# Performance work log

Hardware: AMD Instinct MI355X
Metric: run time of the kernel (lower is better)

Reference implementation:

```python
import jax, jax.numpy as jnp
import numpy as np

N_HEAD = 8
HEAD_DIM = 64
DIM = 512
INNER = N_HEAD * HEAD_DIM
ATT_THRESHOLD = 1e-4
SCALE = HEAD_DIM ** -0.5


def setup_inputs() -> dict:
    key = jax.random.key(0)
    ks = jax.random.split(key, 7)
    b, n, dn = 2, 2048, 2048
    fr = jax.random.normal(ks[0], (b, n, DIM), dtype=jnp.float32)
    dt = jax.random.normal(ks[1], (b, dn, DIM), dtype=jnp.float32)
    s = DIM ** -0.5
    Wq = jax.random.normal(ks[2], (DIM, INNER), dtype=jnp.float32) * s
    Wk = jax.random.normal(ks[3], (DIM, INNER), dtype=jnp.float32) * s
    Wv = jax.random.normal(ks[4], (DIM, INNER), dtype=jnp.float32) * s
    Wo = jax.random.normal(ks[5], (INNER, DIM), dtype=jnp.float32) * (INNER ** -0.5)
    bo = jax.random.normal(ks[6], (DIM,), dtype=jnp.float32) * 0.01
    return {"fr": fr, "dt": dt, "Wq": Wq, "Wk": Wk, "Wv": Wv, "Wo": Wo, "bo": bo}


def reference(fr, dt, Wq, Wk, Wv, Wo, bo):
    b, n, _ = fr.shape
    dn = dt.shape[1]
    # projections -> [b, seq, n_head, head_dim]
    q = (fr @ Wq).reshape(b, n, N_HEAD, HEAD_DIM)
    k = (dt @ Wk).reshape(b, dn, N_HEAD, HEAD_DIM)
    v = (dt @ Wv).reshape(b, dn, N_HEAD, HEAD_DIM)
    # full attention matrix [b, h, n, dn]
    scores = jnp.einsum('bihd,bjhd->bhij', q, k) * SCALE
    attn = jax.nn.softmax(scores, axis=-1)
    # torch .clip(t) with one positional arg clamps the MIN: max(attn, t)
    attn = jnp.maximum(attn, ATT_THRESHOLD) - ATT_THRESHOLD
    attn = attn / jnp.sum(attn, axis=-1, keepdims=True)
    out = jnp.einsum('bhij,bjhd->bihd', attn, v).reshape(b, n, INNER)
    return out @ Wo + bo
```

## Files before the change

kernel.cpp:

```cpp
#include <hip/hip_runtime.h>
#include <hip/hip_bf16.h>

#define BB 2
#define SEQ 2048
#define NHEAD 8
#define HD 64
#define ATT_T 1e-4f
#define QSCALE 0.18033688011112042f

typedef short s16x8 __attribute__((ext_vector_type(8)));
typedef float f32x16 __attribute__((ext_vector_type(16)));

#define MFMA32(a, b, c) __builtin_amdgcn_mfma_f32_32x32x16_bf16((a), (b), (c), 0, 0, 0)
#define EXP2(x) __builtin_amdgcn_exp2f(x)
#define SB0() __builtin_amdgcn_sched_barrier(0)
#define WAITVM0() __builtin_amdgcn_s_waitcnt(0x0F70)
#define WAITVM4() __builtin_amdgcn_s_waitcnt(0x0F74)
#define WAITVM8() __builtin_amdgcn_s_waitcnt(0x0F78)

__device__ __forceinline__ unsigned short bfr(float x) {
  __hip_bfloat16 h = __float2bfloat16(x);
  return __builtin_bit_cast(unsigned short, h);
}
__device__ __forceinline__ unsigned int packbf(float a, float b) {
  return (unsigned int)bfr(a) | ((unsigned int)bfr(b) << 16);
}
__device__ __forceinline__ unsigned int permpack(float a, float b) {
  return __builtin_amdgcn_perm(__builtin_bit_cast(unsigned int, b),
                               __builtin_bit_cast(unsigned int, a), 0x07060302u);
}
__device__ __forceinline__ void async16(const void* g, void* l) {
  __builtin_amdgcn_global_load_lds(
      (const __attribute__((address_space(1))) unsigned int*)g,
      (__attribute__((address_space(3))) unsigned int*)l, 16, 0, 0);
}
__device__ __forceinline__ void plswap(unsigned a, unsigned b, int lh,
                                       unsigned& x, unsigned& z) {
#if __has_builtin(__builtin_amdgcn_permlane32_swap)
  typedef unsigned uint2v __attribute__((ext_vector_type(2)));
  uint2v r = __builtin_amdgcn_permlane32_swap(a, b, false, false);
  x = r[0];
  z = r[1];
#else
  unsigned ea = (unsigned)__shfl_xor((int)a, 32);
  unsigned eb = (unsigned)__shfl_xor((int)b, 32);
  x = lh ? eb : a;
  z = lh ? b : ea;
#endif
}

__global__ __launch_bounds__(256) void convT(const float* __restrict__ w0,
                                             const float* __restrict__ w1,
                                             const float* __restrict__ w2,
                                             const float* __restrict__ w3,
                                             unsigned short* __restrict__ o0,
                                             unsigned short* __restrict__ o1,
                                             unsigned short* __restrict__ o2,
                                             unsigned short* __restrict__ o3) {
  __shared__ float tle[64][65];
  const float* W = blockIdx.z == 0 ? w0 : blockIdx.z == 1 ? w1 : blockIdx.z == 2 ? w2 : w3;
  unsigned short* WT = blockIdx.z == 0 ? o0 : blockIdx.z == 1 ? o1 : blockIdx.z == 2 ? o2 : o3;
  const int r0 = blockIdx.y * 64, c0 = blockIdx.x * 64;
  const int tr = threadIdx.x >> 4;
  const int tc = threadIdx.x & 15;
  #pragma unroll
  for (int i = 0; i < 4; i++) {
    int r = tr + i * 16;
    float4 v = *(const float4*)(W + (size_t)(r0 + r) * 512 + c0 + tc * 4);
    tle[r][tc * 4 + 0] = v.x;
    tle[r][tc * 4 + 1] = v.y;
    tle[r][tc * 4 + 2] = v.z;
    tle[r][tc * 4 + 3] = v.w;
  }
  __syncthreads();
  #pragma unroll
  for (int i = 0; i < 4; i++) {
    int c = tr + i * 16;
    int rr = tc * 4;
    uint2 p;
    p.x = packbf(tle[rr + 0][c], tle[rr + 1][c]);
    p.y = packbf(tle[rr + 2][c], tle[rr + 3][c]);
    *(uint2*)(WT + (size_t)(c0 + c) * 512 + r0 + rr) = p;
  }
}

__global__ __launch_bounds__(256) void gemm_qkv(const float* __restrict__ frF,
                                                const float* __restrict__ dtF,
                                                const unsigned short* __restrict__ WqT,
                                                const unsigned short* __restrict__ WkT,
                                                const unsigned short* __restrict__ WvT,
                                                unsigned short* __restrict__ Qp,
                                                unsigned short* __restrict__ Kp,
                                                unsigned short* __restrict__ VTp) {
  __shared__ __align__(16) unsigned short smem[24576];
  unsigned short* Asm = smem;
  unsigned short* Bsm = smem + 8192;
  const int tid = threadIdx.x, lane = tid & 63, w = tid >> 6;
  const int l31 = lane & 31, lh = lane >> 5;
  const int m0 = blockIdx.y * 64, n0 = blockIdx.x * 128;
  const int z = blockIdx.z;
  const float* A = z == 0 ? frF : dtF;
  const unsigned short* BT = z == 0 ? WqT : (z == 1 ? WkT : WvT);
  unsigned short* OP = z == 0 ? Qp : (z == 1 ? Kp : VTp);
  const float scale = z == 0 ? QSCALE : 1.0f;

  const int arow = tid >> 2, aseg = tid & 3;
  const float* Ap = A + (size_t)(m0 + arow) * 512 + aseg * 16;
  const int aoff = (arow >> 5) * 2048 + aseg * 512 + (arow & 31) * 8;

  auto stageB = [&](int kt, int buf) {
    const int k0 = kt * 64;
    #pragma unroll
    for (int i = 0; i < 4; i++) {
      int r = w * 4 + i, gn = r >> 2, ks = r & 3;
      async16(BT + (size_t)(n0 + gn * 32 + l31) * 512 + k0 + ks * 16 + lh * 8,
              Bsm + buf * 8192 + r * 512);
    }
  };
  auto ldA = [&](int kt, float4* r4) {
    #pragma unroll
    for (int i = 0; i < 4; i++) r4[i] = *(const float4*)(Ap + kt * 64 + i * 4);
  };
  auto wrA = [&](int buf, const float4* r4) {
    uint4 w0v, w1v;
    w0v.x = packbf(r4[0].x, r4[0].y); w0v.y = packbf(r4[0].z, r4[0].w);
    w0v.z = packbf(r4[1].x, r4[1].y); w0v.w = packbf(r4[1].z, r4[1].w);
    w1v.x = packbf(r4[2].x, r4[2].y); w1v.y = packbf(r4[2].z, r4[2].w);
    w1v.z = packbf(r4[3].x, r4[3].y); w1v.w = packbf(r4[3].z, r4[3].w);
    *(uint4*)(Asm + buf * 4096 + aoff) = w0v;
    *(uint4*)(Asm + buf * 4096 + aoff + 256) = w1v;
  };

  f32x16 acc[2];
  #pragma unroll
  for (int j = 0; j < 2; j++)
    #pragma unroll
    for (int r = 0; r < 16; r++) acc[j][r] = 0.f;

  float4 areg[4];
  ldA(0, areg);
  stageB(0, 0);
  wrA(0, areg);
  ldA(1, areg);

  for (int kt = 0; kt < 8; ++kt) {
    __syncthreads();
    if (kt + 1 < 8) {
      const int nb = (kt + 1) & 1;
      stageB(kt + 1, nb);
      wrA(nb, areg);
      if (kt + 2 < 8) ldA(kt + 2, areg);
    }
    const int buf = kt & 1;
    const unsigned short* as = Asm + buf * 4096 + (w & 1) * 2048;
    const unsigned short* bs = Bsm + buf * 8192 + (w >> 1) * 4096;
    #pragma unroll
    for (int ks = 0; ks < 4; ++ks) {
      s16x8 af = *(const s16x8*)(as + ks * 512 + lane * 8);
      s16x8 b0 = *(const s16x8*)(bs + ks * 512 + lane * 8);
      s16x8 b1 = *(const s16x8*)(bs + 2048 + ks * 512 + lane * 8);
      acc[0] = MFMA32(af, b0, acc[0]);
      acc[1] = MFMA32(af, b1, acc[1]);
    }
  }

  const int wm = (w & 1) * 32, wn = (w >> 1) * 64;
  const int bb = m0 >> 11, s0 = m0 & 2047;
  __syncthreads();
  if (z <= 1) {
    #pragma unroll
    for (int j = 0; j < 2; j++)
      #pragma unroll
      for (int r = 0; r < 16; r++) {
        int mm = wm + (r & 3) + 8 * (r >> 2) + 4 * lh;
        int nn = wn + j * 32 + l31;
        smem[mm * 136 + nn] = bfr(acc[j][r] * scale);
      }
    __syncthreads();
    #pragma unroll
    for (int it = 0; it < 4; ++it) {
      int c = tid + it * 256;
      int mm = c >> 4, seg = c & 15;
      uint4 vdat = *(const uint4*)(smem + mm * 136 + seg * 8);
      int n = n0 + seg * 8, h = n >> 6, d = n & 63;
      *(uint4*)(OP + ((size_t)((bb * NHEAD + h) * SEQ + s0 + mm)) * HD + d) = vdat;
    }
  } else {
    #pragma unroll
    for (int j = 0; j < 2; j++)
      #pragma unroll
      for (int r = 0; r < 16; r += 2) {
        int mm = wm + (r & 3) + 8 * (r >> 2) + 4 * lh;
        int nn = wn + j * 32 + l31;
        *(unsigned int*)(smem + nn * 72 + mm) = packbf(acc[j][r], acc[j][r + 1]);
      }
    __syncthreads();
    #pragma unroll
    for (int it = 0; it < 4; ++it) {
      int c = tid + it * 256;
      int nn = c >> 3, seg = c & 7;
      uint4 vdat = *(const uint4*)(smem + nn * 72 + seg * 8);
      int n = n0 + nn, h = n >> 6, d = n & 63;
      *(uint4*)(OP + ((size_t)((bb * NHEAD + h) * HD + d)) * SEQ + s0 + seg * 8) = vdat;
    }
  }
}

__global__ __launch_bounds__(256) void gemm_out(const unsigned short* __restrict__ A,
                                                const unsigned short* __restrict__ BT,
                                                const float* __restrict__ bias,
                                                float* __restrict__ O) {
  __shared__ __align__(16) unsigned short smem[16384];
  unsigned short* Asm = smem;
  unsigned short* Bsm = smem + 8192;
  const int tid = threadIdx.x, lane = tid & 63, w = tid >> 6;
  const int l31 = lane & 31, lh = lane >> 5;
  const int m0 = blockIdx.y * 64, n0 = blockIdx.x * 64;

  auto stage = [&](int kt, int buf) {
    const int k0 = kt * 64;
    #pragma unroll
    for (int i = 0; i < 2; i++) {
      int r = w * 2 + i, g = r >> 2, ks = r & 3;
      async16(A + (size_t)(m0 + g * 32 + l31) * 512 + k0 + ks * 16 + lh * 8,
              Asm + buf * 4096 + r * 512);
      async16(BT + (size_t)(n0 + g * 32 + l31) * 512 + k0 + ks * 16 + lh * 8,
              Bsm + buf * 4096 + r * 512);
    }
  };

  f32x16 acc;
  #pragma unroll
  for (int r = 0; r < 16; r++) acc[r] = 0.f;

  stage(0, 0);
  for (int kt = 0; kt < 8; ++kt) {
    __syncthreads();
    if (kt + 1 < 8) stage(kt + 1, (kt + 1) & 1);
    const int buf = kt & 1;
    const unsigned short* as = Asm + buf * 4096 + (w & 1) * 2048;
    const unsigned short* bs = Bsm + buf * 4096 + (w >> 1) * 2048;
    #pragma unroll
    for (int ks = 0; ks < 4; ++ks) {
      s16x8 af = *(const s16x8*)(as + ks * 512 + lane * 8);
      s16x8 bf = *(const s16x8*)(bs + ks * 512 + lane * 8);
      acc = MFMA32(af, bf, acc);
    }
  }

  const int wm = (w & 1) * 32, wn = (w >> 1) * 32;
  float bv = bias[n0 + wn + l31];
  #pragma unroll
  for (int r = 0; r < 16; r++) {
    int mm = wm + (r & 3) + 8 * (r >> 2) + 4 * lh;
    O[(size_t)(m0 + mm) * 512 + n0 + wn + l31] = acc[r] + bv;
  }
}

__global__ __launch_bounds__(256, 2) void attn_mfma(const unsigned short* __restrict__ Q,
                                                    const unsigned short* __restrict__ K,
                                                    const unsigned short* __restrict__ VT,
                                                    unsigned short* __restrict__ O) {
  __shared__ __align__(16) unsigned short arena[4][4096];
  __shared__ float larr[4][64];
  __shared__ float warr[4][64];

  const int tid = threadIdx.x;
  const int lane = tid & 63;
  const int w = tid >> 6;
  const int l31 = lane & 31, lh = lane >> 5;

  const int bid = blockIdx.x;
  const int g = bid & 7, j = bid >> 3;
  const int bh = g * 2 + (j >> 5);
  const int qt = j & 31;

  const unsigned short* Qh = Q + (size_t)bh * SEQ * HD;
  const unsigned short* Kh = K + (size_t)bh * SEQ * HD;
  const unsigned short* VTh = VT + (size_t)bh * HD * SEQ;

  s16x8 qf[2][4];
  #pragma unroll
  for (int q2 = 0; q2 < 2; q2++)
    #pragma unroll
    for (int t = 0; t < 4; t++)
      qf[q2][t] = *(const s16x8*)(Qh + (size_t)(qt * 64 + q2 * 32 + l31) * HD + 16 * t + 8 * lh);

  unsigned short* kbuf = &arena[w][0];
  const int kbase = w * 512;

  auto stageK = [&](int c, int slot) {
    const unsigned short* base = Kh + (size_t)(kbase + c * 32 + l31) * HD + lh * 8;
    #pragma unroll
    for (int tt = 0; tt < 4; tt++)
      async16(base + tt * 16, kbuf + slot * 2048 + tt * 512);
  };

  f32x16 scp[2];
  auto qkt = [&](int slot) {
    s16x8 kf[4];
    #pragma unroll
    for (int tt = 0; tt < 4; tt++)
      kf[tt] = *(const s16x8*)(kbuf + slot * 2048 + tt * 512 + lane * 8);
    #pragma unroll
    for (int q2 = 0; q2 < 2; q2++) {
      f32x16 sc;
      #pragma unroll
      for (int r = 0; r < 16; r++) sc[r] = 0.f;
      #pragma unroll
      for (int tt = 0; tt < 4; tt++) sc = MFMA32(kf[tt], qf[q2][tt], sc);
      scp[q2] = sc;
    }
  };

  float lsum[2] = {0.f, 0.f};
  auto accum_l = [&]() {
    #pragma unroll
    for (int q2 = 0; q2 < 2; q2++) {
      float s0 = 0.f, s1 = 0.f, s2 = 0.f, s3 = 0.f;
      #pragma unroll
      for (int r = 0; r < 4; r++) {
        s0 += EXP2(scp[q2][r]);
        s1 += EXP2(scp[q2][4 + r]);
        s2 += EXP2(scp[q2][8 + r]);
        s3 += EXP2(scp[q2][12 + r]);
      }
      lsum[q2] += (s0 + s1) + (s2 + s3);
    }
  };

  stageK(0, 0);
  for (int c = 0; c < 16; ++c) {
    const int slot = c & 1;
    if (c + 1 < 16) stageK(c + 1, slot ^ 1);
    if (c > 0) accum_l();
    if (c + 1 < 16) { WAITVM4(); } else { WAITVM0(); }
    SB0();
    qkt(slot);
  }
  accum_l();
  #pragma unroll
  for (int q2 = 0; q2 < 2; q2++) lsum[q2] += __shfl_xor(lsum[q2], 32);
  if (lh == 0) { larr[w][l31] = lsum[0]; larr[w][32 + l31] = lsum[1]; }
  __syncthreads();
  float tl[2];
  #pragma unroll
  for (int q2 = 0; q2 < 2; q2++)
    tl[q2] = ATT_T * (larr[0][q2 * 32 + l31] + larr[1][q2 * 32 + l31] +
                      larr[2][q2 * 32 + l31] + larr[3][q2 * 32 + l31]);

  f32x16 acc[2][2];
  #pragma unroll
  for (int q2 = 0; q2 < 2; q2++)
    #pragma unroll
    for (int dh = 0; dh < 2; dh++)
      #pragma unroll
      for (int r = 0; r < 16; r++) acc[q2][dh][r] = 0.f;
  float wacc[2] = {0.f, 0.f};
  s16x8 vrA[4], vrB[4];

  auto loadV = [&](int c, s16x8(&vr)[4]) {
    #pragma unroll
    for (int dh = 0; dh < 2; dh++)
      #pragma unroll
      for (int kc = 0; kc < 2; kc++)
        vr[dh * 2 + kc] = *(const s16x8*)(VTh + (size_t)(dh * 32 + l31) * SEQ +
                                          kbase + c * 32 + kc * 16 + lh * 8);
  };
  auto softmax_pv = [&](const s16x8(&vr)[4]) {
    s16x8 pf[2][2];
    #pragma unroll
    for (int q2 = 0; q2 < 2; q2++) {
      uint2 quads[4];
      #pragma unroll
      for (int gq = 0; gq < 4; gq++) {
        float u0 = fmaxf(EXP2(scp[q2][4 * gq + 0]) - tl[q2], 0.f);
        float u1 = fmaxf(EXP2(scp[q2][4 * gq + 1]) - tl[q2], 0.f);
        float u2 = fmaxf(EXP2(scp[q2][4 * gq + 2]) - tl[q2], 0.f);
        float u3 = fmaxf(EXP2(scp[q2][4 * gq + 3]) - tl[q2], 0.f);
        wacc[q2] += (u0 + u1) + (u2 + u3);
        quads[gq].x = permpack(u0, u1);
        quads[gq].y = permpack(u2, u3);
      }
      #pragma unroll
      for (int tp = 0; tp < 2; tp++) {
        unsigned x0, z0, x1, z1;
        plswap(quads[2 * tp].x, quads[2 * tp + 1].x, lh, x0, z0);
        plswap(quads[2 * tp].y, quads[2 * tp + 1].y, lh, x1, z1);
        uint4 fr;
        fr.x = x0; fr.y = x1; fr.z = z0; fr.w = z1;
        pf[q2][tp] = __builtin_bit_cast(s16x8, fr);
      }
    }
    #pragma unroll
    for (int q2 = 0; q2 < 2; q2++)
      #pragma unroll
      for (int dh = 0; dh < 2; dh++) {
        acc[q2][dh] = MFMA32(pf[q2][0], vr[dh * 2 + 0], acc[q2][dh]);
        acc[q2][dh] = MFMA32(pf[q2][1], vr[dh * 2 + 1], acc[q2][dh]);
      }
  };

  stageK(0, 0);
  loadV(0, vrA);
  for (int cc = 0; cc < 16; cc += 2) {
    if (cc > 0) softmax_pv(vrB);
    stageK(cc + 1, 1);
    loadV(cc + 1, vrB);
    WAITVM8();
    SB0();
    qkt(0);
    softmax_pv(vrA);
    if (cc + 2 < 16) {
      stageK(cc + 2, 0);
      loadV(cc + 2, vrA);
      WAITVM8();
    } else {
      WAITVM0();
    }
    SB0();
    qkt(1);
  }
  softmax_pv(vrB);

  #pragma unroll
  for (int q2 = 0; q2 < 2; q2++) wacc[q2] += __shfl_xor(wacc[q2], 32);
  if (lh == 0) { warr[w][l31] = wacc[0]; warr[w][32 + l31] = wacc[1]; }
  __syncthreads();

  float* plane0 = (float*)&arena[0][0];
  float* plane1 = (float*)&arena[2][0];

  if (w >= 2) {
    float* pl = (w == 2) ? plane0 : plane1;
    #pragma unroll
    for (int q2 = 0; q2 < 2; q2++)
      #pragma unroll
      for (int dh = 0; dh < 2; dh++)
        #pragma unroll
        for (int r = 0; r < 16; r++) {
          int ql = q2 * 32 + (r & 3) + 8 * (r >> 2) + 4 * lh;
          pl[ql * 64 + dh * 32 + l31] = acc[q2][dh][r];
        }
  }
  __syncthreads();
  if (w < 2) {
    float* pl = (w == 0) ? plane0 : plane1;
    #pragma unroll
    for (int q2 = 0; q2 < 2; q2++)
      #pragma unroll
      for (int dh = 0; dh < 2; dh++)
        #pragma unroll
        for (int r = 0; r < 16; r++) {
          int ql = q2 * 32 + (r & 3) + 8 * (r >> 2) + 4 * lh;
          acc[q2][dh][r] += pl[ql * 64 + dh * 32 + l31];
        }
  }
  __syncthreads();
  if (w == 1) {
    #pragma unroll
    for (int q2 = 0; q2 < 2; q2++)
      #pragma unroll
      for (int dh = 0; dh < 2; dh++)
        #pragma unroll
        for (int r = 0; r < 16; r++) {
          int ql = q2 * 32 + (r & 3) + 8 * (r >> 2) + 4 * lh;
          plane0[ql * 64 + dh * 32 + l31] = acc[q2][dh][r];
        }
  }
  __syncthreads();
  unsigned short* otile = &arena[2][0];
  if (w == 0) {
    #pragma unroll
    for (int q2 = 0; q2 < 2; q2++)
      #pragma unroll
      for (int dh = 0; dh < 2; dh++)
        #pragma unroll
        for (int r = 0; r < 16; r++) {
          int ql = q2 * 32 + (r & 3) + 8 * (r >> 2) + 4 * lh;
          float wt = warr[0][ql] + warr[1][ql] + warr[2][ql] + warr[3][ql];
          float v = (acc[q2][dh][r] + plane0[ql * 64 + dh * 32 + l31]) / wt;
          otile[ql * 64 + dh * 32 + l31] = bfr(v);
        }
  }
  __syncthreads();
  const int b = bh >> 3, h = bh & 7;
  #pragma unroll
  for (int it = 0; it < 2; ++it) {
    int c2 = tid + it * 256;
    int mm = c2 >> 3, seg = c2 & 7;
    uint4 vdat = *(const uint4*)(otile + mm * 64 + seg * 8);
    *(uint4*)(O + ((size_t)(b * SEQ + qt * 64 + mm)) * 512 + h * HD + seg * 8) = vdat;
  }
}

extern "C" void kernel_launch(void* const* d_in, const int* in_sizes, int n_in,
                              void* d_out, int out_size, void* d_ws, size_t ws_size,
                              hipStream_t stream) {
  const float* fr = (const float*)d_in[0];
  const float* dt = (const float*)d_in[1];
  const float* Wq = (const float*)d_in[2];
  const float* Wk = (const float*)d_in[3];
  const float* Wv = (const float*)d_in[4];
  const float* Wo = (const float*)d_in[5];
  const float* bo = (const float*)d_in[6];
  float* out = (float*)d_out;

  const size_t planeE = (size_t)BB * SEQ * 512;
  const size_t wE = 512 * 512;
  unsigned short* p = (unsigned short*)d_ws;
  unsigned short* WqT = p; p += wE;
  unsigned short* WkT = p; p += wE;
  unsigned short* WvT = p; p += wE;
  unsigned short* WoT = p; p += wE;
  unsigned short* Qp  = p; p += planeE;
  unsigned short* Kp  = p; p += planeE;
  unsigned short* VTp = p; p += planeE;
  unsigned short* aoB = p; p += planeE;

  convT<<<dim3(8, 8, 4), 256, 0, stream>>>(Wq, Wk, Wv, Wo, WqT, WkT, WvT, WoT);

  gemm_qkv<<<dim3(4, 64, 3), 256, 0, stream>>>(fr, dt, WqT, WkT, WvT, Qp, Kp, VTp);

  attn_mfma<<<BB * NHEAD * 32, 256, 0, stream>>>(Qp, Kp, VTp, aoB);

  gemm_out<<<dim3(8, 64), 256, 0, stream>>>(aoB, WoT, bo, out);
}
```

Baseline: 162.4 us.

## Pre-convert fr/dt to bf16 in prep kernel and async-stage A in QKV GEMM

The weight-transpose kernel becomes a combined prep kernel that also converts the fr and dt activations to bf16, writing them into the output buffer as scratch space. The QKV GEMM then loads A tiles with direct async global-to-LDS copies, the same way it loads B, instead of loading fp32 into registers, packing, and writing to LDS. This removes register pressure and the conversion work inside the GEMM loop, and the V projection no longer re-reads dt in fp32. In exchange there is an extra write and read of the bf16 activation planes. Reusing d_out as scratch is safe only because gemm_out writes the output later.

```diff
diff --git a/kernel.cpp b/kernel.cpp
--- a/kernel.cpp
+++ b/kernel.cpp
@@ -49,18 +49,40 @@
 #endif
 }
 
-__global__ __launch_bounds__(256) void convT(const float* __restrict__ w0,
-                                             const float* __restrict__ w1,
-                                             const float* __restrict__ w2,
-                                             const float* __restrict__ w3,
-                                             unsigned short* __restrict__ o0,
-                                             unsigned short* __restrict__ o1,
-                                             unsigned short* __restrict__ o2,
-                                             unsigned short* __restrict__ o3) {
+__global__ __launch_bounds__(256) void prep(const float* __restrict__ fr,
+                                            const float* __restrict__ dt,
+                                            const float* __restrict__ w0,
+                                            const float* __restrict__ w1,
+                                            const float* __restrict__ w2,
+                                            const float* __restrict__ w3,
+                                            unsigned short* __restrict__ frB,
+                                            unsigned short* __restrict__ dtB,
+                                            unsigned short* __restrict__ o0,
+                                            unsigned short* __restrict__ o1,
+                                            unsigned short* __restrict__ o2,
+                                            unsigned short* __restrict__ o3) {
+  const int bid = blockIdx.x;
+  if (bid < 2048) {
+    const float* src = (bid < 1024) ? fr : dt;
+    unsigned short* dst = (bid < 1024) ? frB : dtB;
+    const int chunk = (bid < 1024) ? bid : bid - 1024;
+    const size_t base = (size_t)chunk * 2048 + threadIdx.x * 8;
+    float4 a = *(const float4*)(src + base);
+    float4 b = *(const float4*)(src + base + 4);
+    uint4 o;
+    o.x = packbf(a.x, a.y);
+    o.y = packbf(a.z, a.w);
+    o.z = packbf(b.x, b.y);
+    o.w = packbf(b.z, b.w);
+    *(uint4*)(dst + base) = o;
+    return;
+  }
   __shared__ float tle[64][65];
-  const float* W = blockIdx.z == 0 ? w0 : blockIdx.z == 1 ? w1 : blockIdx.z == 2 ? w2 : w3;
-  unsigned short* WT = blockIdx.z == 0 ? o0 : blockIdx.z == 1 ? o1 : blockIdx.z == 2 ? o2 : o3;
-  const int r0 = blockIdx.y * 64, c0 = blockIdx.x * 64;
+  const int t = bid - 2048;
+  const int z = t >> 6, by = (t >> 3) & 7, bx = t & 7;
+  const float* W = z == 0 ? w0 : z == 1 ? w1 : z == 2 ? w2 : w3;
+  unsigned short* WT = z == 0 ? o0 : z == 1 ? o1 : z == 2 ? o2 : o3;
+  const int r0 = by * 64, c0 = bx * 64;
   const int tr = threadIdx.x >> 4;
   const int tc = threadIdx.x & 15;
   #pragma unroll
@@ -84,8 +106,8 @@
   }
 }
 
-__global__ __launch_bounds__(256) void gemm_qkv(const float* __restrict__ frF,
-                                                const float* __restrict__ dtF,
+__global__ __launch_bounds__(256) void gemm_qkv(const unsigned short* __restrict__ frB,
+                                                const unsigned short* __restrict__ dtB,
                                                 const unsigned short* __restrict__ WqT,
                                                 const unsigned short* __restrict__ WkT,
                                                 const unsigned short* __restrict__ WvT,
@@ -99,17 +121,19 @@
   const int l31 = lane & 31, lh = lane >> 5;
   const int m0 = blockIdx.y * 64, n0 = blockIdx.x * 128;
   const int z = blockIdx.z;
-  const float* A = z == 0 ? frF : dtF;
+  const unsigned short* Ab = z == 0 ? frB : dtB;
   const unsigned short* BT = z == 0 ? WqT : (z == 1 ? WkT : WvT);
   unsigned short* OP = z == 0 ? Qp : (z == 1 ? Kp : VTp);
   const float scale = z == 0 ? QSCALE : 1.0f;
 
-  const int arow = tid >> 2, aseg = tid & 3;
-  const float* Ap = A + (size_t)(m0 + arow) * 512 + aseg * 16;
-  const int aoff = (arow >> 5) * 2048 + aseg * 512 + (arow & 31) * 8;
-
-  auto stageB = [&](int kt, int buf) {
+  auto stage = [&](int kt, int buf) {
     const int k0 = kt * 64;
+    #pragma unroll
+    for (int i = 0; i < 2; i++) {
+      int r = w * 2 + i, g = r >> 2, ks = r & 3;
+      async16(Ab + (size_t)(m0 + g * 32 + l31) * 512 + k0 + ks * 16 + lh * 8,
+              Asm + buf * 4096 + r * 512);
+    }
     #pragma unroll
     for (int i = 0; i < 4; i++) {
       int r = w * 4 + i, gn = r >> 2, ks = r & 3;
@@ -117,19 +141,6 @@
               Bsm + buf * 8192 + r * 512);
     }
   };
-  auto ldA = [&](int kt, float4* r4) {
-    #pragma unroll
-    for (int i = 0; i < 4; i++) r4[i] = *(const float4*)(Ap + kt * 64 + i * 4);
-  };
-  auto wrA = [&](int buf, const float4* r4) {
-    uint4 w0v, w1v;
-    w0v.x = packbf(r4[0].x, r4[0].y); w0v.y = packbf(r4[0].z, r4[0].w);
-    w0v.z = packbf(r4[1].x, r4[1].y); w0v.w = packbf(r4[1].z, r4[1].w);
-    w1v.x = packbf(r4[2].x, r4[2].y); w1v.y = packbf(r4[2].z, r4[2].w);
-    w1v.z = packbf(r4[3].x, r4[3].y); w1v.w = packbf(r4[3].z, r4[3].w);
-    *(uint4*)(Asm + buf * 4096 + aoff) = w0v;
-    *(uint4*)(Asm + buf * 4096 + aoff + 256) = w1v;
-  };
 
   f32x16 acc[2];
   #pragma unroll
@@ -137,20 +148,10 @@
     #pragma unroll
     for (int r = 0; r < 16; r++) acc[j][r] = 0.f;
 
-  float4 areg[4];
-  ldA(0, areg);
-  stageB(0, 0);
-  wrA(0, areg);
-  ldA(1, areg);
-
+  stage(0, 0);
   for (int kt = 0; kt < 8; ++kt) {
     __syncthreads();
-    if (kt + 1 < 8) {
-      const int nb = (kt + 1) & 1;
-      stageB(kt + 1, nb);
-      wrA(nb, areg);
-      if (kt + 2 < 8) ldA(kt + 2, areg);
-    }
+    if (kt + 1 < 8) stage(kt + 1, (kt + 1) & 1);
     const int buf = kt & 1;
     const unsigned short* as = Asm + buf * 4096 + (w & 1) * 2048;
     const unsigned short* bs = Bsm + buf * 8192 + (w >> 1) * 4096;
@@ -518,9 +519,12 @@
   unsigned short* VTp = p; p += planeE;
   unsigned short* aoB = p; p += planeE;
 
-  convT<<<dim3(8, 8, 4), 256, 0, stream>>>(Wq, Wk, Wv, Wo, WqT, WkT, WvT, WoT);
-
-  gemm_qkv<<<dim3(4, 64, 3), 256, 0, stream>>>(fr, dt, WqT, WkT, WvT, Qp, Kp, VTp);
+  unsigned short* frB = (unsigned short*)d_out;
+  unsigned short* dtB = (unsigned short*)d_out + planeE;
+
+  prep<<<2304, 256, 0, stream>>>(fr, dt, Wq, Wk, Wv, Wo, frB, dtB, WqT, WkT, WvT, WoT);
+
+  gemm_qkv<<<dim3(4, 64, 3), 256, 0, stream>>>(frB, dtB, WqT, WkT, WvT, Qp, Kp, VTp);
 
   attn_mfma<<<BB * NHEAD * 32, 256, 0, stream>>>(Qp, Kp, VTp, aoB);
 
```

Measured after the change: 164.0 us. About the same (+1.0%).
